# Performance work log

Hardware: AMD Instinct MI355X
Metric: run time of the kernel (lower is better)

The kernel has to match this reference:

```python
import jax, jax.numpy as jnp
import numpy as np

B, T, C = 2, 2048, 1024
NH = 16
DFF = 4096
EPS = 1e-5


def setup_inputs() -> dict:
    key = jax.random.key(0)
    ks = jax.random.split(key, 12)
    s = 0.02
    return {
        "x": jax.random.normal(ks[0], (B, T, C), dtype=jnp.float32),
        "Wq": jax.random.normal(ks[1], (C, C), dtype=jnp.float32) * s,
        "bq": jax.random.normal(ks[2], (C,), dtype=jnp.float32) * s,
        "Wk": jax.random.normal(ks[3], (C, C), dtype=jnp.float32) * s,
        "bk": jax.random.normal(ks[4], (C,), dtype=jnp.float32) * s,
        "Wv": jax.random.normal(ks[5], (C, C), dtype=jnp.float32) * s,
        "bv": jax.random.normal(ks[6], (C,), dtype=jnp.float32) * s,
        "W1": jax.random.normal(ks[7], (C, DFF), dtype=jnp.float32) * s,
        "b1": jax.random.normal(ks[8], (DFF,), dtype=jnp.float32) * s,
        "W2": jax.random.normal(ks[9], (DFF, C), dtype=jnp.float32) * s,
        "b2": jax.random.normal(ks[10], (C,), dtype=jnp.float32) * s,
        "ln_w": jnp.ones((C,), dtype=jnp.float32),
    }


def _layernorm(x, w):
    # LayerNorm over last dim, weight only (bias=False), eps=1e-5
    mu = jnp.mean(x, axis=-1, keepdims=True)
    var = jnp.mean(jnp.square(x - mu), axis=-1, keepdims=True)
    return (x - mu) / jnp.sqrt(var + EPS) * w


def reference(x, Wq, bq, Wk, bk, Wv, bv, W1, b1, W2, b2, ln_w):
    Bx, Tx, Cx = x.shape
    hd = Cx // NH
    q = (x @ Wq + bq).reshape(Bx, Tx, NH, hd).transpose(0, 2, 1, 3)  # [B,H,T,hd]
    k = (x @ Wk + bk).reshape(Bx, Tx, NH, hd).transpose(0, 2, 1, 3)
    v = (x @ Wv + bv).reshape(Bx, Tx, NH, hd).transpose(0, 2, 1, 3)
    # NOTE: original scales by sqrt(d_k) = sqrt(FULL model dim C), not head dim
    scores = jnp.einsum("bhqd,bhkd->bhqk", q, k) / jnp.sqrt(jnp.float32(Cx))
    causal = jnp.tril(jnp.ones((Tx, Tx), dtype=bool))
    scores = jnp.where(causal[None, None, :, :], scores, -jnp.inf)
    attn = jax.nn.softmax(scores, axis=-1)
    head_out = jnp.einsum("bhqk,bhkd->bhqd", attn, v)
    a = head_out.transpose(0, 2, 1, 3).reshape(Bx, Tx, Cx)
    # residuals: out = x + ln(x) with SHARED ln weight
    h = a + _layernorm(a, ln_w)
    f = jax.nn.relu(h @ W1 + b1) @ W2 + b2
    out = f + _layernorm(f, ln_w)
    return out
```

## Files before the change

kernel.cpp:

```cpp
#include <hip/hip_runtime.h>
#include <math.h>


typedef __attribute__((ext_vector_type(8))) short short8;
typedef __attribute__((ext_vector_type(4))) float f32x4;

__device__ __forceinline__ unsigned short f2bf(float f) {
    unsigned u = __builtin_bit_cast(unsigned, f);
    unsigned r = u + 0x7fffu + ((u >> 16) & 1u);
    return (unsigned short)(r >> 16);
}

__global__ __launch_bounds__(256) void prep_kernel(
    const float* __restrict__ x,  const float* __restrict__ Wq,
    const float* __restrict__ Wk, const float* __restrict__ Wv,
    const float* __restrict__ W1, const float* __restrict__ W2,
    const float* __restrict__ bq, const float* __restrict__ bk,
    unsigned short* __restrict__ x_bf,  unsigned short* __restrict__ Wqk_t,
    unsigned short* __restrict__ Wvt,   unsigned short* __restrict__ W1t,
    unsigned short* __restrict__ W2t,   float* __restrict__ bqk)
{
    const int bid = blockIdx.x;
    const int tid = threadIdx.x;

    if (bid < 4096) {
        const int i = (bid * 256 + tid) * 4;
        float4 v = *(const float4*)(x + i);
        ushort4 o;
        o.x = f2bf(v.x); o.y = f2bf(v.y); o.z = f2bf(v.z); o.w = f2bf(v.w);
        *(ushort4*)(x_bf + i) = o;
        return;
    }
    if (bid >= 6912) {
        const int i = (bid - 6912) * 256 + tid;
        bqk[i] = i < 1024 ? bq[i] : bk[i - 1024];
        return;
    }

    __shared__ float tile[64][65];
    const float* src; unsigned short* dst; int K, N, t;
    if (bid < 4352)      { t = bid - 4096; src = Wq; dst = Wqk_t;           K = 1024; N = 1024; }
    else if (bid < 4608) { t = bid - 4352; src = Wk; dst = Wqk_t + 1048576; K = 1024; N = 1024; }
    else if (bid < 4864) { t = bid - 4608; src = Wv; dst = Wvt;             K = 1024; N = 1024; }
    else if (bid < 5888) { t = bid - 4864; src = W1; dst = W1t;             K = 1024; N = 4096; }
    else                 { t = bid - 5888; src = W2; dst = W2t;             K = 4096; N = 1024; }

    const int ncols = N >> 6;
    const int n0 = (t % ncols) * 64;
    const int k0 = (t / ncols) * 64;
    const int tx = tid & 15;
    const int ty = tid >> 4;
#pragma unroll
    for (int i = 0; i < 4; ++i) {
        const int r = ty + i * 16;
        float4 v = *(const float4*)(src + (size_t)(k0 + r) * N + n0 + tx * 4);
        tile[r][tx * 4 + 0] = v.x;
        tile[r][tx * 4 + 1] = v.y;
        tile[r][tx * 4 + 2] = v.z;
        tile[r][tx * 4 + 3] = v.w;
    }
    __syncthreads();
#pragma unroll
    for (int i = 0; i < 4; ++i) {
        const int n = ty + i * 16;
        ushort4 o;
        o.x = f2bf(tile[tx * 4 + 0][n]);
        o.y = f2bf(tile[tx * 4 + 1][n]);
        o.z = f2bf(tile[tx * 4 + 2][n]);
        o.w = f2bf(tile[tx * 4 + 3][n]);
        *(ushort4*)(dst + (size_t)(n0 + n) * K + k0 + tx * 4) = o;
    }
}

template <int TM, int TN>
__device__ __forceinline__ void gemm_body(
    unsigned short* As, unsigned short* Bs,
    const unsigned short* __restrict__ A, const unsigned short* __restrict__ Bt,
    const float* __restrict__ bias, float* __restrict__ Cf,
    unsigned short* __restrict__ Cb, int M, int N, int K, int mode,
    int bx, int by, int kbeg, int kend)
{
    constexpr int NI   = TM / 32;
    constexpr int NJ   = TN / 32;
    constexpr int NPA  = TM / 8;
    constexpr int NPB  = TN / 8;
    constexpr int MAXA = (NPA + 3) / 4;
    constexpr int MAXB = (NPB + 3) / 4;
    constexpr int ASZ  = TM * 64;
    constexpr int BSZ  = TN * 64;
    constexpr int LPW  = (NPA + NPB) / 4;

    const int tid  = threadIdx.x;
    const int lane = tid & 63;
    const int w    = tid >> 6;
    const int wm   = (w & 1) * (TM / 2);
    const int wn   = (w >> 1) * (TN / 2);
    const int fm   = lane & 15;
    const int quad = lane >> 4;

    const int row0 = by * TM;
    const int col0 = bx * TN;

    const int srow = lane >> 3;
    const int scol = ((lane & 7) ^ srow) << 3;

    const unsigned short* aptr[MAXA];
    int aoff[MAXA];
#pragma unroll
    for (int i = 0; i < MAXA; ++i) {
        const int p = w + i * 4;
        if (p < NPA) {
            aptr[i] = A + (size_t)(row0 + p * 8 + srow) * K + scol;
            aoff[i] = p * 8 * 64;
        }
    }
    const unsigned short* bptr[MAXB];
    int boff[MAXB];
#pragma unroll
    for (int i = 0; i < MAXB; ++i) {
        const int p = w + i * 4;
        if (p < NPB) {
            bptr[i] = Bt + (size_t)(col0 + p * 8 + srow) * K + scol;
            boff[i] = p * 8 * 64;
        }
    }

    auto stage = [&](int k0, unsigned short* Ab, unsigned short* Bb) {
#pragma unroll
        for (int i = 0; i < MAXA; ++i)
            if (w + i * 4 < NPA)
                __builtin_amdgcn_global_load_lds(
                    (const __attribute__((address_space(1))) void*)(aptr[i] + k0),
                    (__attribute__((address_space(3))) void*)&Ab[aoff[i]], 16, 0, 0);
#pragma unroll
        for (int i = 0; i < MAXB; ++i)
            if (w + i * 4 < NPB)
                __builtin_amdgcn_global_load_lds(
                    (const __attribute__((address_space(1))) void*)(bptr[i] + k0),
                    (__attribute__((address_space(3))) void*)&Bb[boff[i]], 16, 0, 0);
    };

    f32x4 acc[NI][NJ] = {};

    stage(kbeg, As, Bs);
    const int NT = (kend - kbeg) >> 6;

    for (int t = 0; t < NT; ++t) {
        unsigned short* Ac = As + (t & 1) * ASZ;
        unsigned short* Bc = Bs + (t & 1) * BSZ;

        if (t + 1 < NT) {
            stage(kbeg + (t + 1) * 64, As + ((t + 1) & 1) * ASZ,
                                       Bs + ((t + 1) & 1) * BSZ);
            asm volatile("s_waitcnt vmcnt(%0)" :: "n"(LPW) : "memory");
        } else {
            asm volatile("s_waitcnt vmcnt(0)" ::: "memory");
        }
        __builtin_amdgcn_s_barrier();

#pragma unroll
        for (int kh = 0; kh < 2; ++kh) {
            short8 af[NI], bf[NJ];
#pragma unroll
            for (int i = 0; i < NI; ++i) {
                const int r = wm + i * 16 + fm;
                const int sl = ((kh << 2) | quad) ^ (r & 7);
                af[i] = *(const short8*)&Ac[r * 64 + sl * 8];
            }
#pragma unroll
            for (int j = 0; j < NJ; ++j) {
                const int r = wn + j * 16 + fm;
                const int sl = ((kh << 2) | quad) ^ (r & 7);
                bf[j] = *(const short8*)&Bc[r * 64 + sl * 8];
            }
#pragma unroll
            for (int i = 0; i < NI; ++i)
#pragma unroll
                for (int j = 0; j < NJ; ++j)
                    acc[i][j] = __builtin_amdgcn_mfma_f32_16x16x32_bf16(
                        af[i], bf[j], acc[i][j], 0, 0, 0);
        }

        __builtin_amdgcn_s_barrier();
    }

#pragma unroll
    for (int j = 0; j < NJ; ++j) {
        const int col = col0 + wn + j * 16 + fm;
        const float bcol = (mode == 3 || mode == 4) ? 0.f : bias[col];
#pragma unroll
        for (int i = 0; i < NI; ++i) {
            const int rbase = row0 + wm + i * 16 + quad * 4;
#pragma unroll
            for (int r = 0; r < 4; ++r) {
                const int row = rbase + r;
                float val = acc[i][j][r] + ((mode == 3) ? bias[row] : bcol);
                if (mode == 1) val = fmaxf(val, 0.f);
                if (mode == 0 || mode == 4) Cf[(size_t)row * N + col] = val;
                else                        Cb[(size_t)row * N + col] = f2bf(val);
            }
        }
    }
}

template <int TM, int TN>
__global__ __launch_bounds__(256) void gemm_bf16_mfma(
    const unsigned short* __restrict__ A, const unsigned short* __restrict__ Bt,
    const float* __restrict__ bias, float* __restrict__ Cf,
    unsigned short* __restrict__ Cb, int M, int N, int K, int mode)
{
    __shared__ unsigned short As[2 * TM * 64];
    __shared__ unsigned short Bs[2 * TN * 64];
    gemm_body<TM, TN>(As, Bs, A, Bt, bias, Cf, Cb, M, N, K, mode,
                      blockIdx.x, blockIdx.y, 0, K);
}

template <int TM, int TN>
__global__ __launch_bounds__(256) void gemm_splitk(
    const unsigned short* __restrict__ A, const unsigned short* __restrict__ Bt,
    const float* __restrict__ bias, float* __restrict__ C0,
    float* __restrict__ C1, int M, int N, int K,
    int nxh, int rows_per_xcd_h, int nbh)
{
    __shared__ unsigned short As[2 * TM * 64];
    __shared__ unsigned short Bs[2 * TN * 64];
    const int half = blockIdx.x >= nbh;
    const int r    = blockIdx.x - (half ? nbh : 0);
    const int xcd  = blockIdx.x & 7;
    const int idx  = r >> 3;
    const int bx   = idx % nxh;
    const int by   = xcd * rows_per_xcd_h + idx / nxh;
    const int kb   = half ? (K >> 1) : 0;
    gemm_body<TM, TN>(As, Bs, A, Bt, bias, half ? C1 : C0, nullptr,
                      M, N, K, half ? 4 : 0, bx, by, kb, kb + (K >> 1));
}

template <int TM, int TN>
__global__ __launch_bounds__(256) void gemm_dual(
    const unsigned short* __restrict__ A0, const unsigned short* __restrict__ B0,
    const float* __restrict__ bias0, unsigned short* __restrict__ C0,
    int M0, int N0, int K0, int mode0, int nb0, int nx0,
    const unsigned short* __restrict__ A1, const unsigned short* __restrict__ B1,
    const float* __restrict__ bias1, unsigned short* __restrict__ C1,
    int M1, int N1, int K1, int mode1, int nx1)
{
    __shared__ unsigned short As[2 * TM * 64];
    __shared__ unsigned short Bs[2 * TN * 64];
    const int bid = blockIdx.x;
    if (bid < nb0) {
        gemm_body<TM, TN>(As, Bs, A0, B0, bias0, nullptr, C0,
                          M0, N0, K0, mode0, bid % nx0, bid / nx0, 0, K0);
    } else {
        const int t = bid - nb0;
        gemm_body<TM, TN>(As, Bs, A1, B1, bias1, nullptr, C1,
                          M1, N1, K1, mode1, t % nx1, t / nx1, 0, K1);
    }
}

__global__ __launch_bounds__(256) void fattn_mfma(
    const unsigned short* __restrict__ qk,
    const unsigned short* __restrict__ vt,
    float* __restrict__ a)
{
    const int T = 2048, LDQK = 2048, LDVT = 4096, OUTC = 1024;
    const float cs = 0.04508422f;

    __shared__ unsigned short Qs[64 * 64];
    __shared__ unsigned short Ks[64 * 64];
    __shared__ unsigned short Vs[64 * 64];
    __shared__ unsigned short Ps[4][16][72];

    const int tid  = threadIdx.x;
    const int lane = tid & 63;
    const int w    = tid >> 6;
    const int fm   = lane & 15;
    const int quad = lane >> 4;
    const int srow = lane >> 3;
    const int scol = ((lane & 7) ^ srow) << 3;

    const int n  = blockIdx.x;
    const int lo = n & 255, hi = n >> 8;
    const int h  = ((lo >> 5) & 7) | ((hi & 1) << 3);
    const int b  = hi >> 1;
    const int qv = lo & 31;
    const int u  = ((qv & 1) << 4) | ((qv & 2) << 2) | (qv & 4) |
                   ((qv & 8) >> 2) | ((qv & 16) >> 4);
    const int qb = (hi & 1) ? (31 - u) : u;
    const int q0 = qb * 64;

    const size_t rowbase = (size_t)b * T;

#pragma unroll
    for (int i = 0; i < 2; ++i) {
        const int p = w * 2 + i;
        const unsigned short* src = qk + (rowbase + q0 + p * 8 + srow) * LDQK
                                       + h * 64 + scol;
        __builtin_amdgcn_global_load_lds(
            (const __attribute__((address_space(1))) void*)src,
            (__attribute__((address_space(3))) void*)&Qs[p * 8 * 64], 16, 0, 0);
    }
    __syncthreads();
    const int qr = w * 16 + fm;
    short8 qf0 = *(const short8*)&Qs[qr * 64 + ((quad ^ (qr & 7)) << 3)];
    short8 qf1 = *(const short8*)&Qs[qr * 64 + (((4 | quad) ^ (qr & 7)) << 3)];

    short8 ones;
#pragma unroll
    for (int i = 0; i < 8; ++i) ones[i] = (short)0x3F80;

    f32x4 o[4] = {};
    f32x4 lacc = {};

    const int qglob = q0 + w * 16 + fm;

    for (int jt = 0; jt <= qb; ++jt) {
        const int j0 = jt * 64;
        __syncthreads();
#pragma unroll
        for (int i = 0; i < 4; ++i) {
            const int unit = w * 4 + i;
            if (unit < 8) {
                const unsigned short* ksrc = qk + (rowbase + j0 + unit * 8 + srow) * LDQK
                                                + 1024 + h * 64 + scol;
                __builtin_amdgcn_global_load_lds(
                    (const __attribute__((address_space(1))) void*)ksrc,
                    (__attribute__((address_space(3))) void*)&Ks[unit * 8 * 64], 16, 0, 0);
            } else {
                const int p = unit - 8;
                const unsigned short* vsrc = vt + (size_t)(h * 64 + p * 8 + srow) * LDVT
                                                + rowbase + j0 + scol;
                __builtin_amdgcn_global_load_lds(
                    (const __attribute__((address_space(1))) void*)vsrc,
                    (__attribute__((address_space(3))) void*)&Vs[p * 8 * 64], 16, 0, 0);
            }
        }
        __syncthreads();

        f32x4 s[4];
#pragma unroll
        for (int j = 0; j < 4; ++j) {
            const int r = j * 16 + fm;
            short8 k0 = *(const short8*)&Ks[r * 64 + ((quad ^ (r & 7)) << 3)];
            short8 k1 = *(const short8*)&Ks[r * 64 + (((4 | quad) ^ (r & 7)) << 3)];
            f32x4 acc = {};
            acc = __builtin_amdgcn_mfma_f32_16x16x32_bf16(k0, qf0, acc, 0, 0, 0);
            acc = __builtin_amdgcn_mfma_f32_16x16x32_bf16(k1, qf1, acc, 0, 0, 0);
            s[j] = acc;
        }

        if (jt == qb) {
#pragma unroll
            for (int j = 0; j < 4; ++j) {
                const int kbase = j0 + j * 16 + quad * 4;
#pragma unroll
                for (int r = 0; r < 4; ++r) {
                    const float e = exp2f(s[j][r] * cs);
                    s[j][r] = (kbase + r > qglob) ? 0.f : e;
                }
            }
        } else {
#pragma unroll
            for (int j = 0; j < 4; ++j)
#pragma unroll
                for (int r = 0; r < 4; ++r)
                    s[j][r] = exp2f(s[j][r] * cs);
        }

#pragma unroll
        for (int j = 0; j < 4; ++j) {
            unsigned d0, d1;
            asm("v_cvt_pk_bf16_f32 %0, %1, %2"
                : "=v"(d0) : "v"(s[j][0]), "v"(s[j][1]));
            asm("v_cvt_pk_bf16_f32 %0, %1, %2"
                : "=v"(d1) : "v"(s[j][2]), "v"(s[j][3]));
            *(uint2*)&Ps[w][fm][j * 16 + quad * 4] = make_uint2(d0, d1);
        }
        short8 pf0 = *(const short8*)&Ps[w][fm][quad * 8];
        short8 pf1 = *(const short8*)&Ps[w][fm][32 + quad * 8];

#pragma unroll
        for (int jd = 0; jd < 4; ++jd) {
            const int r = jd * 16 + fm;
            short8 v0 = *(const short8*)&Vs[r * 64 + ((quad ^ (r & 7)) << 3)];
            short8 v1 = *(const short8*)&Vs[r * 64 + (((4 | quad) ^ (r & 7)) << 3)];
            o[jd] = __builtin_amdgcn_mfma_f32_16x16x32_bf16(pf0, v0, o[jd], 0, 0, 0);
            o[jd] = __builtin_amdgcn_mfma_f32_16x16x32_bf16(pf1, v1, o[jd], 0, 0, 0);
        }
        lacc = __builtin_amdgcn_mfma_f32_16x16x32_bf16(pf0, ones, lacc, 0, 0, 0);
        lacc = __builtin_amdgcn_mfma_f32_16x16x32_bf16(pf1, ones, lacc, 0, 0, 0);
    }

    const size_t orow = rowbase + q0 + w * 16 + quad * 4;
#pragma unroll
    for (int r = 0; r < 4; ++r) {
        const float inv = 1.0f / lacc[r];
#pragma unroll
        for (int jd = 0; jd < 4; ++jd)
            a[(orow + r) * OUTC + h * 64 + jd * 16 + fm] = o[jd][r] * inv;
    }
}

__global__ __launch_bounds__(256) void add_ln_kernel(
    const float* __restrict__ in, const float* __restrict__ in2,
    const float* __restrict__ w,
    float* __restrict__ outf, unsigned short* __restrict__ outb, int bf16_out)
{
    const int C = 1024;
    const int row = blockIdx.x;
    const int tid = threadIdx.x;
    const int lane = tid & 63;
    const int wv   = tid >> 6;

    __shared__ float red[8];

    float4 xv = *(const float4*)(in + (size_t)row * C + tid * 4);
    if (in2) {
        float4 yv = *(const float4*)(in2 + (size_t)row * C + tid * 4);
        xv.x += yv.x; xv.y += yv.y; xv.z += yv.z; xv.w += yv.w;
    }

    float s = xv.x + xv.y + xv.z + xv.w;
#pragma unroll
    for (int o = 32; o > 0; o >>= 1) s += __shfl_xor(s, o, 64);
    if (lane == 0) red[wv] = s;
    __syncthreads();
    const float mu = (red[0] + red[1] + red[2] + red[3]) * (1.0f / 1024.0f);

    float dx = xv.x - mu, dy = xv.y - mu, dz = xv.z - mu, dw = xv.w - mu;
    float v = dx * dx + dy * dy + dz * dz + dw * dw;
#pragma unroll
    for (int o = 32; o > 0; o >>= 1) v += __shfl_xor(v, o, 64);
    if (lane == 0) red[4 + wv] = v;
    __syncthreads();
    const float rstd = rsqrtf((red[4] + red[5] + red[6] + red[7]) * (1.0f / 1024.0f)
                              + 1e-5f);

    float4 wvv = *(const float4*)(w + tid * 4);
    float ox = xv.x + dx * rstd * wvv.x;
    float oy = xv.y + dy * rstd * wvv.y;
    float oz = xv.z + dz * rstd * wvv.z;
    float ow = xv.w + dw * rstd * wvv.w;
    if (bf16_out) {
        ushort4 o4;
        o4.x = f2bf(ox); o4.y = f2bf(oy); o4.z = f2bf(oz); o4.w = f2bf(ow);
        *(ushort4*)(outb + (size_t)row * C + tid * 4) = o4;
    } else {
        *(float4*)(outf + (size_t)row * C + tid * 4) = make_float4(ox, oy, oz, ow);
    }
}

extern "C" void kernel_launch(void* const* d_in, const int* in_sizes, int n_in,
                              void* d_out, int out_size, void* d_ws, size_t ws_size,
                              hipStream_t stream)
{
    const float* x    = (const float*)d_in[0];
    const float* Wq   = (const float*)d_in[1];
    const float* bq   = (const float*)d_in[2];
    const float* Wk   = (const float*)d_in[3];
    const float* bk   = (const float*)d_in[4];
    const float* Wv   = (const float*)d_in[5];
    const float* bv   = (const float*)d_in[6];
    const float* W1   = (const float*)d_in[7];
    const float* b1   = (const float*)d_in[8];
    const float* W2   = (const float*)d_in[9];
    const float* b2   = (const float*)d_in[10];
    const float* ln_w = (const float*)d_in[11];
    float* out = (float*)d_out;
    char* ws = (char*)d_ws;

    const int B = 2, T = 2048, C = 1024, DFF = 4096;
    const int M = B * T;
    const size_t MB = 1048576;

    unsigned short* qk_bf = (unsigned short*)(ws);
    unsigned short* vt_bf = (unsigned short*)(ws + 16 * MB);
    float*          a     = (float*)(ws + 24 * MB);
    unsigned short* x_bf  = (unsigned short*)(ws + 40 * MB);
    unsigned short* Wqk_t = (unsigned short*)(ws + 48 * MB);
    unsigned short* Wvt   = (unsigned short*)(ws + 52 * MB);
    unsigned short* W1t   = (unsigned short*)(ws + 54 * MB);
    unsigned short* W2t   = (unsigned short*)(ws + 62 * MB);
    float*          bqk   = (float*)(ws + 70 * MB);
    unsigned short* u_bf  = (unsigned short*)(ws + 71 * MB);
    unsigned short* h_bf  = x_bf;
    float*          f     = (float*)(ws);
    float*          f2    = a;

    dim3 blk(256);

    prep_kernel<<<dim3(6920), blk, 0, stream>>>(
        x, Wq, Wk, Wv, W1, W2, bq, bk,
        x_bf, Wqk_t, Wvt, W1t, W2t, bqk);

    gemm_dual<64, 128><<<dim3(1536), blk, 0, stream>>>(
        x_bf, Wqk_t, bqk, qk_bf, M, 2 * C, C, 2, 1024, 16,
        Wvt, x_bf, bv, vt_bf, C, M, C, 3, 32);

    fattn_mfma<<<dim3(1024), blk, 0, stream>>>(qk_bf, vt_bf, a);

    add_ln_kernel<<<dim3(M), blk, 0, stream>>>(a, nullptr, ln_w, nullptr, h_bf, 1);

    gemm_bf16_mfma<64, 128><<<dim3(DFF / 128, M / 64), blk, 0, stream>>>(
        h_bf, W1t, b1, nullptr, u_bf, M, DFF, C, 1);

    gemm_splitk<128, 64><<<dim3(1024), blk, 0, stream>>>(
        u_bf, W2t, b2, f, f2, M, C, DFF, 16, 4, 512);

    add_ln_kernel<<<dim3(M), blk, 0, stream>>>(f, f2, ln_w, out, nullptr, 0);
}
```

Before: 339.8 us.

## Use single-buffer GEMM for dual/splitk, double-buffer 128x128 for FFN1, add setprio

Adds a single-buffered GEMM body with explicit syncthreads and switches the QKV dual GEMM and the split-K FFN2 GEMM to it. Halving their LDS footprint is meant to raise occupancy, at the cost of losing load/compute overlap. The double-buffered path is kept as gemm_body_db and used for FFN1 with a larger 128x128 tile for more operand reuse. s_setprio is also wrapped around the MFMA sections in the attention kernel so matrix work gets issue priority over other waves.

```diff
diff --git a/kernel.cpp b/kernel.cpp
--- a/kernel.cpp
+++ b/kernel.cpp
@@ -79,6 +79,117 @@
     const float* __restrict__ bias, float* __restrict__ Cf,
     unsigned short* __restrict__ Cb, int M, int N, int K, int mode,
     int bx, int by, int kbeg, int kend)
+{
+    constexpr int NI   = TM / 32;
+    constexpr int NJ   = TN / 32;
+    constexpr int NPA  = TM / 8;
+    constexpr int NPB  = TN / 8;
+    constexpr int MAXA = (NPA + 3) / 4;
+    constexpr int MAXB = (NPB + 3) / 4;
+
+    const int tid  = threadIdx.x;
+    const int lane = tid & 63;
+    const int w    = tid >> 6;
+    const int wm   = (w & 1) * (TM / 2);
+    const int wn   = (w >> 1) * (TN / 2);
+    const int fm   = lane & 15;
+    const int quad = lane >> 4;
+
+    const int row0 = by * TM;
+    const int col0 = bx * TN;
+
+    const int srow = lane >> 3;
+    const int scol = ((lane & 7) ^ srow) << 3;
+
+    const unsigned short* aptr[MAXA];
+    int aoff[MAXA];
+#pragma unroll
+    for (int i = 0; i < MAXA; ++i) {
+        const int p = w + i * 4;
+        if (p < NPA) {
+            aptr[i] = A + (size_t)(row0 + p * 8 + srow) * K + scol;
+            aoff[i] = p * 8 * 64;
+        }
+    }
+    const unsigned short* bptr[MAXB];
+    int boff[MAXB];
+#pragma unroll
+    for (int i = 0; i < MAXB; ++i) {
+        const int p = w + i * 4;
+        if (p < NPB) {
+            bptr[i] = Bt + (size_t)(col0 + p * 8 + srow) * K + scol;
+            boff[i] = p * 8 * 64;
+        }
+    }
+
+    f32x4 acc[NI][NJ] = {};
+
+    for (int k0 = kbeg; k0 < kend; k0 += 64) {
+        __syncthreads();
+#pragma unroll
+        for (int i = 0; i < MAXA; ++i)
+            if (w + i * 4 < NPA)
+                __builtin_amdgcn_global_load_lds(
+                    (const __attribute__((address_space(1))) void*)(aptr[i] + k0),
+                    (__attribute__((address_space(3))) void*)&As[aoff[i]], 16, 0, 0);
+#pragma unroll
+        for (int i = 0; i < MAXB; ++i)
+            if (w + i * 4 < NPB)
+                __builtin_amdgcn_global_load_lds(
+                    (const __attribute__((address_space(1))) void*)(bptr[i] + k0),
+                    (__attribute__((address_space(3))) void*)&Bs[boff[i]], 16, 0, 0);
+        __syncthreads();
+
+#pragma unroll
+        for (int kh = 0; kh < 2; ++kh) {
+            short8 af[NI], bf[NJ];
+#pragma unroll
+            for (int i = 0; i < NI; ++i) {
+                const int r = wm + i * 16 + fm;
+                const int sl = ((kh << 2) | quad) ^ (r & 7);
+                af[i] = *(const short8*)&As[r * 64 + sl * 8];
+            }
+#pragma unroll
+            for (int j = 0; j < NJ; ++j) {
+                const int r = wn + j * 16 + fm;
+                const int sl = ((kh << 2) | quad) ^ (r & 7);
+                bf[j] = *(const short8*)&Bs[r * 64 + sl * 8];
+            }
+#pragma unroll
+            for (int i = 0; i < NI; ++i)
+#pragma unroll
+                for (int j = 0; j < NJ; ++j)
+                    acc[i][j] = __builtin_amdgcn_mfma_f32_16x16x32_bf16(
+                        af[i], bf[j], acc[i][j], 0, 0, 0);
+        }
+    }
+
+#pragma unroll
+    for (int j = 0; j < NJ; ++j) {
+        const int col = col0 + wn + j * 16 + fm;
+        const float bcol = (mode == 3 || mode == 4) ? 0.f : bias[col];
+#pragma unroll
+        for (int i = 0; i < NI; ++i) {
+            const int rbase = row0 + wm + i * 16 + quad * 4;
+#pragma unroll
+            for (int r = 0; r < 4; ++r) {
+                const int row = rbase + r;
+                float val = acc[i][j][r] + ((mode == 3) ? bias[row] : bcol);
+                if (mode == 1) val = fmaxf(val, 0.f);
+                if (mode == 0 || mode == 4) Cf[(size_t)row * N + col] = val;
+                else                        Cb[(size_t)row * N + col] = f2bf(val);
+            }
+        }
+    }
+}
+
+template <int TM, int TN>
+__device__ __forceinline__ void gemm_body_db(
+    unsigned short* As, unsigned short* Bs,
+    const unsigned short* __restrict__ A, const unsigned short* __restrict__ Bt,
+    const float* __restrict__ bias, float* __restrict__ Cf,
+    unsigned short* __restrict__ Cb, int M, int N, int K, int mode,
+    int bx, int by)
 {
     constexpr int NI   = TM / 32;
     constexpr int NJ   = TN / 32;
@@ -142,16 +253,16 @@
 
     f32x4 acc[NI][NJ] = {};
 
-    stage(kbeg, As, Bs);
-    const int NT = (kend - kbeg) >> 6;
+    stage(0, As, Bs);
+    const int NT = K >> 6;
 
     for (int t = 0; t < NT; ++t) {
         unsigned short* Ac = As + (t & 1) * ASZ;
         unsigned short* Bc = Bs + (t & 1) * BSZ;
 
         if (t + 1 < NT) {
-            stage(kbeg + (t + 1) * 64, As + ((t + 1) & 1) * ASZ,
-                                       Bs + ((t + 1) & 1) * BSZ);
+            stage((t + 1) * 64, As + ((t + 1) & 1) * ASZ,
+                                Bs + ((t + 1) & 1) * BSZ);
             asm volatile("s_waitcnt vmcnt(%0)" :: "n"(LPW) : "memory");
         } else {
             asm volatile("s_waitcnt vmcnt(0)" ::: "memory");
@@ -204,15 +315,15 @@
 }
 
 template <int TM, int TN>
-__global__ __launch_bounds__(256) void gemm_bf16_mfma(
+__global__ __launch_bounds__(256) void gemm_db(
     const unsigned short* __restrict__ A, const unsigned short* __restrict__ Bt,
     const float* __restrict__ bias, float* __restrict__ Cf,
     unsigned short* __restrict__ Cb, int M, int N, int K, int mode)
 {
     __shared__ unsigned short As[2 * TM * 64];
     __shared__ unsigned short Bs[2 * TN * 64];
-    gemm_body<TM, TN>(As, Bs, A, Bt, bias, Cf, Cb, M, N, K, mode,
-                      blockIdx.x, blockIdx.y, 0, K);
+    gemm_body_db<TM, TN>(As, Bs, A, Bt, bias, Cf, Cb, M, N, K, mode,
+                         blockIdx.x, blockIdx.y);
 }
 
 template <int TM, int TN>
@@ -222,8 +333,8 @@
     float* __restrict__ C1, int M, int N, int K,
     int nxh, int rows_per_xcd_h, int nbh)
 {
-    __shared__ unsigned short As[2 * TM * 64];
-    __shared__ unsigned short Bs[2 * TN * 64];
+    __shared__ unsigned short As[TM * 64];
+    __shared__ unsigned short Bs[TN * 64];
     const int half = blockIdx.x >= nbh;
     const int r    = blockIdx.x - (half ? nbh : 0);
     const int xcd  = blockIdx.x & 7;
@@ -244,8 +355,8 @@
     const float* __restrict__ bias1, unsigned short* __restrict__ C1,
     int M1, int N1, int K1, int mode1, int nx1)
 {
-    __shared__ unsigned short As[2 * TM * 64];
-    __shared__ unsigned short Bs[2 * TN * 64];
+    __shared__ unsigned short As[TM * 64];
+    __shared__ unsigned short Bs[TN * 64];
     const int bid = blockIdx.x;
     if (bid < nb0) {
         gemm_body<TM, TN>(As, Bs, A0, B0, bias0, nullptr, C0,
@@ -336,6 +447,7 @@
         }
         __syncthreads();
 
+        __builtin_amdgcn_s_setprio(1);
         f32x4 s[4];
 #pragma unroll
         for (int j = 0; j < 4; ++j) {
@@ -347,6 +459,7 @@
             acc = __builtin_amdgcn_mfma_f32_16x16x32_bf16(k1, qf1, acc, 0, 0, 0);
             s[j] = acc;
         }
+        __builtin_amdgcn_s_setprio(0);
 
         if (jt == qb) {
 #pragma unroll
@@ -378,6 +491,7 @@
         short8 pf0 = *(const short8*)&Ps[w][fm][quad * 8];
         short8 pf1 = *(const short8*)&Ps[w][fm][32 + quad * 8];
 
+        __builtin_amdgcn_s_setprio(1);
 #pragma unroll
         for (int jd = 0; jd < 4; ++jd) {
             const int r = jd * 16 + fm;
@@ -388,6 +502,7 @@
         }
         lacc = __builtin_amdgcn_mfma_f32_16x16x32_bf16(pf0, ones, lacc, 0, 0, 0);
         lacc = __builtin_amdgcn_mfma_f32_16x16x32_bf16(pf1, ones, lacc, 0, 0, 0);
+        __builtin_amdgcn_s_setprio(0);
     }
 
     const size_t orow = rowbase + q0 + w * 16 + quad * 4;
@@ -500,7 +615,7 @@
 
     add_ln_kernel<<<dim3(M), blk, 0, stream>>>(a, nullptr, ln_w, nullptr, h_bf, 1);
 
-    gemm_bf16_mfma<64, 128><<<dim3(DFF / 128, M / 64), blk, 0, stream>>>(
+    gemm_db<128, 128><<<dim3(DFF / 128, M / 128), blk, 0, stream>>>(
         h_bf, W1t, b1, nullptr, u_bf, M, DFF, C, 1);
 
     gemm_splitk<128, 64><<<dim3(1024), blk, 0, stream>>>(
```

Measured after the change: 332.8 us. -2.1%, faster.
